# Kernel optimization log

Measured on AMD Instinct MI355X. Metric: run time of the kernel, lower is better.

The kernel has to match this reference:

```python
import jax, jax.numpy as jnp
import numpy as np

NUM_CLASSES = 80
STRIDES = (32, 16, 8)
SCORE_THRESH = 0.01
NMS_THRESH = 0.45
TOP_K = 200
PRE_K = 4096          # pre-NMS candidate cap (greedy NMS only ever emits TOP_K boxes)
NEG = -1e9            # 'suppressed' score sentinel (avoids -inf NaN issues)
CLS_OFFSET = 4096.0   # class-aware NMS: offset boxes per class (boxes live in [0, 608])

_ANCHORS_PX = [[(116, 90), (156, 198), (373, 326)],
               [(30, 61), (62, 45), (59, 119)],
               [(10, 13), (16, 30), (33, 23)]]


def setup_inputs() -> dict:
    key = jax.random.key(0)
    bs, img = 8, 608
    inp = {}
    for lvl, (stride, anc) in enumerate(zip(STRIDES, _ANCHORS_PX)):
        H = W = img // stride
        key, k = jax.random.split(key)
        inp[f"in{lvl}"] = jax.random.normal(k, (bs, 3 * (NUM_CLASSES + 5), H, W), dtype=jnp.float32)
        aw = jnp.array([a[0] / stride for a in anc], jnp.float32)
        ah = jnp.array([a[1] / stride for a in anc], jnp.float32)
        inp[f"aw{lvl}"] = jnp.broadcast_to(aw[None, :, None, None], (bs, 3, H, W))
        inp[f"ah{lvl}"] = jnp.broadcast_to(ah[None, :, None, None], (bs, 3, H, W))
        inp[f"gx{lvl}"] = jnp.broadcast_to(jnp.arange(W, dtype=jnp.float32)[None, None, None, :], (bs, 3, H, W))
        inp[f"gy{lvl}"] = jnp.broadcast_to(jnp.arange(H, dtype=jnp.float32)[None, None, :, None], (bs, 3, H, W))
    return inp


def _decode_level(x, aw, ah, gx, gy, stride):
    bs, _, H, W = x.shape
    x = x.reshape(bs, -1, NUM_CLASSES + 5, H, W).transpose(0, 1, 3, 4, 2)  # [bs,3,H,W,85]
    px = jax.nn.sigmoid(x[..., 0]) + gx
    py = jax.nn.sigmoid(x[..., 1]) + gy
    pw = jnp.exp(x[..., 2]) * aw
    ph = jnp.exp(x[..., 3]) * ah
    conf = jax.nn.sigmoid(x[..., 4])
    cls = jax.nn.sigmoid(x[..., 5:])
    boxes = jnp.stack([px, py, pw, ph], -1) * jnp.float32(stride)  # [bs,3,H,W,4] (cx,cy,w,h)
    return boxes.reshape(bs, -1, 4), conf.reshape(bs, -1), cls.reshape(bs, -1, NUM_CLASSES)


def _center_to_corner(b):
    cx, cy, w, h = b[..., 0], b[..., 1], b[..., 2], b[..., 3]
    return jnp.stack([cx - w / 2, cy - h / 2, cx + w / 2, cy + h / 2], -1)


def _nms_image(boxes, conf, cls):
    # boxes [N,4] corner, conf [N], cls [N,C]
    N, C = cls.shape
    scores = (conf[:, None] * cls).reshape(-1)                          # [N*C]
    cboxes = jnp.broadcast_to(boxes[:, None, :], (N, C, 4)).reshape(-1, 4)
    labels = jnp.broadcast_to(jnp.arange(C), (N, C)).reshape(-1)
    s = jnp.where(scores > SCORE_THRESH, scores, NEG)
    top_s, idx = jax.lax.top_k(s, PRE_K)
    b = cboxes[idx]                                                     # [PRE_K,4]
    l = labels[idx]
    ob = b + (l.astype(jnp.float32) * CLS_OFFSET)[:, None]              # class-aware offset
    area = (ob[:, 2] - ob[:, 0]) * (ob[:, 3] - ob[:, 1])

    def step(live, _):
        i = jnp.argmax(live)
        si, bi, ai = live[i], ob[i], area[i]
        x1 = jnp.maximum(bi[0], ob[:, 0]); y1 = jnp.maximum(bi[1], ob[:, 1])
        x2 = jnp.minimum(bi[2], ob[:, 2]); y2 = jnp.minimum(bi[3], ob[:, 3])
        inter = jnp.clip(x2 - x1, 0.0) * jnp.clip(y2 - y1, 0.0)
        iou = inter / (ai + area - inter + 1e-9)
        live = jnp.where(iou > NMS_THRESH, NEG, live)                   # suppresses self too
        return live, (i, si)

    _, (sel, sel_s) = jax.lax.scan(step, top_s, None, length=TOP_K)
    valid = sel_s > SCORE_THRESH
    out_b = jnp.where(valid[:, None], b[sel], 0.0)
    out_l = jnp.where(valid, l[sel], 0).astype(jnp.float32)
    out_s = jnp.where(valid, sel_s, 0.0)
    return jnp.concatenate([out_b, out_l[:, None], out_s[:, None]], -1)  # [TOP_K, 6]


def _forward(levels):
    boxes, conf, cls = [], [], []
    for (x, aw, ah, gx, gy), stride in zip(levels, STRIDES):
        bb, cc, cl = _decode_level(x, aw, ah, gx, gy, stride)
        boxes.append(bb); conf.append(cc); cls.append(cl)
    boxes = _center_to_corner(jnp.concatenate(boxes, 1))   # [bs,N,4]
    conf = jnp.concatenate(conf, 1)                        # [bs,N]
    cls = jnp.concatenate(cls, 1)                          # [bs,N,C]
    return jax.vmap(_nms_image)(boxes, conf, cls)          # [bs,TOP_K,6]


def reference(in0, aw0, ah0, gx0, gy0, in1, aw1, ah1, gx1, gy1, in2, aw2, ah2, gx2, gy2):
    levels = [(in0, aw0, ah0, gx0, gy0), (in1, aw1, ah1, gx1, gy1), (in2, aw2, ah2, gx2, gy2)]
    return _forward(levels)
```

## Files before the change

kernel.cpp:

```cpp
#include <hip/hip_runtime.h>
#include <stdint.h>

typedef unsigned int u32;
typedef unsigned long long u64;

#define NCLS 80
#define NBOX 22743
#define PREK 4096
#define BCAP 65536
#define NIMG 8
#define SCORE_TH 0.01f
#define IOU_TH 0.45f
#define TOPK 200

#define DCH 20
#define DNCH 4
#define GCH 10
#define GNCH 8

#define LCAP 1536

#define BKCAP 8
#define HCAP 224
#define HUGE_TH 3488.0f

#define RJC 4
#define RJW 1024

#define CBINS 512
#define CBIN_BASE 7680u

#define HIST_OFF 0
#define CNT_OFF  16384
#define ZERO_BYTES 18432
#define WIN_OFF  18432
#define BND_OFF  280576
#define PART_OFF BND_OFF
#define BOX_OFF  4474880
#define SKEY_OFF 7385984
#define SOBOX_OFF 7648128
#define SAREA_OFF 8172416

__device__ __forceinline__ float sigmf(float x) { return 1.0f / (1.0f + expf(-x)); }

__device__ __forceinline__ u64 pad_key(int i) { return (u64)(~(u32)i); }

__global__ __launch_bounds__(256) void init_k(uint4* __restrict__ ws) {
  const int i = blockIdx.x * 256 + threadIdx.x;
  if (i < ZERO_BYTES / 16) ws[i] = make_uint4(0u, 0u, 0u, 0u);
}

__global__ __launch_bounds__(256) void decode_hist_all(const float* __restrict__ in0,
                              const float* __restrict__ in1, const float* __restrict__ in2,
                              float4* __restrict__ boxes, u32* __restrict__ hist) {
  __shared__ u32 lh[CBINS];
  const int img = blockIdx.y;
  const int c0 = blockIdx.z * DCH;
  for (int i = threadIdx.x; i < CBINS; i += 256) lh[i] = 0;
  __syncthreads();

  const int bx = blockIdx.x;
  if (bx < 5) {
    const int W = 19, HW = 361;
    const int r = bx * 256 + threadIdx.x;
    if (r < 3 * HW) {
      const int a = r / HW, p = r - a * HW;
      const int y = p / W, x = p - y * W;
      const float* base = in0 + ((size_t)(img * 255 + a * 85)) * (size_t)HW + p;
      float l[DCH];
#pragma unroll
      for (int k = 0; k < DCH; ++k) l[k] = base[(size_t)(5 + c0 + k) * HW];
      const float x4 = base[4 * (size_t)HW];
      if (c0 == 0) {
        const float aw = (a == 0) ? 3.625f : ((a == 1) ? 4.875f : 11.65625f);
        const float ah = (a == 0) ? 2.8125f : ((a == 1) ? 6.1875f : 10.1875f);
        const float x0 = base[0];
        const float x1 = base[(size_t)HW];
        const float x2 = base[2 * (size_t)HW];
        const float x3 = base[3 * (size_t)HW];
        const float px = sigmf(x0) + (float)x;
        const float py = sigmf(x1) + (float)y;
        const float pw = expf(x2) * aw;
        const float ph = expf(x3) * ah;
        const float cx = px * 32.f, cy = py * 32.f, bw = pw * 32.f, bh = ph * 32.f;
        boxes[(size_t)img * NBOX + r] =
            make_float4(cx - bw * 0.5f, cy - bh * 0.5f, cx + bw * 0.5f, cy + bh * 0.5f);
      }
      const float conf = sigmf(x4);
      if (conf > SCORE_TH) {
#pragma unroll
        for (int k = 0; k < DCH; ++k) {
          float s = conf * sigmf(l[k]);
          if (s > SCORE_TH) {
            u32 bin = (__float_as_uint(s) >> 17) - CBIN_BASE;
            atomicAdd(&lh[bin], 1u);
          }
        }
      }
    }
  } else {
    const bool L1 = bx < 10;
    const float* in = L1 ? in1 : in2;
    const int W = L1 ? 38 : 76;
    const int HW = L1 ? 1444 : 5776;
    const int lvl_off = L1 ? 1083 : 5415;
    const float stride = L1 ? 16.f : 8.f;
    const int HW4 = HW >> 2;
    const int idx = (bx - (L1 ? 5 : 10)) * 256 + threadIdx.x;
    if (idx < 3 * HW4) {
      const int a = idx / HW4;
      const int p0 = (idx - a * HW4) << 2;
      const float* base = in + ((size_t)(img * 255 + a * 85)) * (size_t)HW + p0;
      float4 scv[DCH];
#pragma unroll
      for (int k = 0; k < DCH; ++k)
        scv[k] = *(const float4*)(base + (size_t)(5 + c0 + k) * HW);
      float4 v4 = *(const float4*)(base + 4 * (size_t)HW);
      const float* t4 = (const float*)&v4;
      float conf[4];
      if (c0 == 0) {
        const float aw = L1 ? ((a == 0) ? 1.875f : ((a == 1) ? 3.875f : 3.6875f))
                            : ((a == 0) ? 1.25f : ((a == 1) ? 2.f : 4.125f));
        const float ah = L1 ? ((a == 0) ? 3.8125f : ((a == 1) ? 2.8125f : 7.4375f))
                            : ((a == 0) ? 1.625f : ((a == 1) ? 3.75f : 2.875f));
        float4 v0 = *(const float4*)(base);
        float4 v1 = *(const float4*)(base + (size_t)HW);
        float4 v2 = *(const float4*)(base + 2 * (size_t)HW);
        float4 v3 = *(const float4*)(base + 3 * (size_t)HW);
        const float* t0 = (const float*)&v0;
        const float* t1 = (const float*)&v1;
        const float* t2 = (const float*)&v2;
        const float* t3 = (const float*)&v3;
        float4* bout = boxes + (size_t)img * NBOX + lvl_off + a * HW + p0;
#pragma unroll
        for (int i = 0; i < 4; ++i) {
          const int p = p0 + i;
          const int y = p / W, x = p - y * W;
          const float px = sigmf(t0[i]) + (float)x;
          const float py = sigmf(t1[i]) + (float)y;
          const float pw = expf(t2[i]) * aw;
          const float ph = expf(t3[i]) * ah;
          const float cx = px * stride, cy = py * stride, bw = pw * stride, bh = ph * stride;
          bout[i] = make_float4(cx - bw * 0.5f, cy - bh * 0.5f, cx + bw * 0.5f, cy + bh * 0.5f);
        }
      }
#pragma unroll
      for (int i = 0; i < 4; ++i) conf[i] = sigmf(t4[i]);
#pragma unroll
      for (int k = 0; k < DCH; ++k) {
        const float* s4 = (const float*)&scv[k];
#pragma unroll
        for (int i = 0; i < 4; ++i) {
          float s = conf[i] * sigmf(s4[i]);
          if (s > SCORE_TH) {
            u32 bin = (__float_as_uint(s) >> 17) - CBIN_BASE;
            atomicAdd(&lh[bin], 1u);
          }
        }
      }
    }
  }
  __syncthreads();
  u32* gh = hist + (size_t)img * CBINS;
  for (int i = threadIdx.x; i < CBINS; i += 256) {
    u32 v = lh[i];
    if (v) atomicAdd(&gh[i], v);
  }
}

__device__ __forceinline__ void flush_list(const u64* llist, int lcnt, int cap,
                                           int* gctr, u64* glist, int gcap) {
  __shared__ int gbase_s;
  int n = lcnt < cap ? lcnt : cap;
  if (threadIdx.x == 0) gbase_s = n ? atomicAdd(gctr, n) : 0;
  __syncthreads();
  const int gb = gbase_s;
  for (int i = threadIdx.x; i < n; i += 256) {
    int pos = gb + i;
    if (pos < gcap) glist[pos] = llist[i];
  }
}

__global__ __launch_bounds__(256) void gather_all(const float* __restrict__ in0,
                         const float* __restrict__ in1, const float* __restrict__ in2,
                         const u32* __restrict__ hist, int* __restrict__ cnt,
                         u64* __restrict__ winners, u64* __restrict__ boundary) {
  __shared__ u64 lwin[LCAP];
  __shared__ u64 lbnd[LCAP];
  __shared__ int lwc, lbc;
  __shared__ u32 s_wsum[4];
  __shared__ int sB;
  const int img = blockIdx.y;
  const int c0 = blockIdx.z * GCH;
  const int t = threadIdx.x;
  if (t == 0) { lwc = 0; lbc = 0; sB = -1; }

  {
    const u32* gh = hist + (size_t)img * CBINS;
    u32 hv0 = gh[t * 2], hv1 = gh[t * 2 + 1];
    u32 s = hv0 + hv1;
    const int lane = t & 63;
    u32 v = s;
#pragma unroll
    for (int off = 1; off < 64; off <<= 1) {
      u32 o = __shfl_down(v, off);
      if (lane + off < 64) v += o;
    }
    if (lane == 0) s_wsum[t >> 6] = v;
    __syncthreads();
    u32 hi = 0;
    for (int w = (t >> 6) + 1; w < 4; ++w) hi += s_wsum[w];
    const u32 above = hi + (v - s);
    if (above < (u32)PREK && above + s >= (u32)PREK) {
      u32 cum = above + hv1;
      if (cum >= (u32)PREK) sB = t * 2 + 1;
      else sB = t * 2;
    }
    __syncthreads();
  }
  const int B = sB;

  int* cw = &cnt[img * 64];
  int* cb = &cnt[img * 64 + 32];
  u64* wl = winners + (size_t)img * PREK;
  u64* bl = boundary + (size_t)img * BCAP;
  const int bx = blockIdx.x;

  if (bx < 5) {
    const int HW = 361;
    const int r = bx * 256 + t;
    if (r < 3 * HW) {
      const int a = r / HW, p = r - a * HW;
      const float* base = in0 + ((size_t)(img * 255 + a * 85)) * (size_t)HW + p;
      const int boxg = r;
      float l[GCH];
#pragma unroll
      for (int k = 0; k < GCH; ++k) l[k] = base[(size_t)(5 + c0 + k) * HW];
      const float conf = sigmf(base[4 * (size_t)HW]);
#pragma unroll
      for (int k = 0; k < GCH; ++k) {
        float s = conf * sigmf(l[k]);
        if (s > SCORE_TH) {
          u32 key = __float_as_uint(s);
          int wbin = (int)((key >> 17) - CBIN_BASE);
          if (wbin >= B) {
            u64 kv = ((u64)key << 32) | (u64)(~(u32)(boxg * NCLS + (c0 + k)));
            if (wbin > B) {
              int p2 = atomicAdd(&lwc, 1);
              if (p2 < LCAP) lwin[p2] = kv;
              else { int g = atomicAdd(cw, 1); if (g < PREK) wl[g] = kv; }
            } else {
              int p2 = atomicAdd(&lbc, 1);
              if (p2 < LCAP) lbnd[p2] = kv;
              else { int g = atomicAdd(cb, 1); if (g < BCAP) bl[g] = kv; }
            }
          }
        }
      }
    }
  } else {
    const bool L1 = bx < 10;
    const float* in = L1 ? in1 : in2;
    const int HW = L1 ? 1444 : 5776;
    const int lvl_off = L1 ? 1083 : 5415;
    const int HW4 = HW >> 2;
    const int idx = (bx - (L1 ? 5 : 10)) * 256 + t;
    if (idx < 3 * HW4) {
      const int a = idx / HW4;
      const int p0 = (idx - a * HW4) << 2;
      const float* base = in + ((size_t)(img * 255 + a * 85)) * (size_t)HW + p0;
      const int boxg0 = lvl_off + a * HW + p0;
      float4 scv[GCH];
#pragma unroll
      for (int k = 0; k < GCH; ++k)
        scv[k] = *(const float4*)(base + (size_t)(5 + c0 + k) * HW);
      float4 v4 = *(const float4*)(base + 4 * (size_t)HW);
      const float* t4 = (const float*)&v4;
      float conf[4];
#pragma unroll
      for (int i = 0; i < 4; ++i) conf[i] = sigmf(t4[i]);
#pragma unroll
      for (int k = 0; k < GCH; ++k) {
        const float* s4 = (const float*)&scv[k];
        const int c = c0 + k;
#pragma unroll
        for (int i = 0; i < 4; ++i) {
          float s = conf[i] * sigmf(s4[i]);
          if (s > SCORE_TH) {
            u32 key = __float_as_uint(s);
            int wbin = (int)((key >> 17) - CBIN_BASE);
            if (wbin >= B) {
              u64 kv = ((u64)key << 32) | (u64)(~(u32)((boxg0 + i) * NCLS + c));
              if (wbin > B) {
                int p = atomicAdd(&lwc, 1);
                if (p < LCAP) lwin[p] = kv;
                else { int g = atomicAdd(cw, 1); if (g < PREK) wl[g] = kv; }
              } else {
                int p = atomicAdd(&lbc, 1);
                if (p < LCAP) lbnd[p] = kv;
                else { int g = atomicAdd(cb, 1); if (g < BCAP) bl[g] = kv; }
              }
            }
          }
        }
      }
    }
  }
  __syncthreads();
  flush_list(lwin, lwc, LCAP, cw, wl, PREK);
  flush_list(lbnd, lbc, LCAP, cb, bl, BCAP);
}

__global__ void resolve_k(const u64* __restrict__ boundary,
                          int* __restrict__ cnt, u64* __restrict__ winners) {
  const int img = blockIdx.x;
  const int cw_pre = cnt[img * 64];
  const int T = PREK - cw_pre;
  int bc = cnt[img * 64 + 32];
  if (bc > BCAP) bc = BCAP;
  if (T <= 0 || bc <= 0) return;
  const u64* bnd = boundary + (size_t)img * BCAP;
  u64* wl = winners + (size_t)img * PREK;
  int* cw = &cnt[img * 64];

  __shared__ u32 h2[16384];
  __shared__ u32 lsum[256];
  __shared__ u32 above[256];
  __shared__ u32 s_total;
  __shared__ int sB2, sT2;
  __shared__ u64 ties[512];
  __shared__ int tcnt;
  __shared__ u64 lw2[PREK];
  __shared__ int lw2c;
  __shared__ int gbase_s;
  const int t = threadIdx.x;
  for (int i = t; i < 16384; i += 256) h2[i] = 0;
  if (t == 0) { tcnt = 0; sB2 = -1; sT2 = 0; lw2c = 0; }
  __syncthreads();
  for (int i = t; i < bc; i += 256) atomicAdd(&h2[(u32)(bnd[i] >> 35) & 0x3FFFu], 1u);
  __syncthreads();
  u32 s = 0;
  for (int j = 0; j < 64; ++j) s += h2[t * 64 + j];
  lsum[t] = s;
  __syncthreads();
  if (t == 0) {
    u32 acc = 0;
    for (int i = 255; i >= 0; --i) { above[i] = acc; acc += lsum[i]; }
    s_total = acc;
  }
  __syncthreads();
  if ((int)s_total > T) {
    if (above[t] < (u32)T && above[t] + lsum[t] >= (u32)T) {
      u32 cum = above[t];
      for (int j = 63; j >= 0; --j) {
        u32 hv = h2[t * 64 + j];
        cum += hv;
        if (cum >= (u32)T) { sB2 = t * 64 + j; sT2 = (int)((u32)T - (cum - hv)); break; }
      }
    }
  }
  __syncthreads();
  const int B2 = sB2, T2 = sT2;
  for (int i = t; i < bc; i += 256) {
    u64 e = bnd[i];
    int low = (int)((u32)(e >> 35) & 0x3FFFu);
    if (low > B2) {
      int p = atomicAdd(&lw2c, 1);
      if (p < PREK) lw2[p] = e;
    } else if (low == B2) {
      int tp = atomicAdd(&tcnt, 1);
      if (tp < 512) ties[tp] = e;
    }
  }
  __syncthreads();
  int n = lw2c < PREK ? lw2c : PREK;
  if (t == 0) gbase_s = n ? atomicAdd(cw, n) : 0;
  __syncthreads();
  for (int i = t; i < n; i += 256) {
    int pos = gbase_s + i;
    if (pos < PREK) wl[pos] = lw2[i];
  }
  __syncthreads();
  if (t == 0 && T2 > 0) {
    int tc = tcnt < 512 ? tcnt : 512;
    for (int k = 0; k < T2 && k < tc; ++k) {
      int bi = -1; u64 bk = 0;
      for (int i = 0; i < tc; ++i)
        if (ties[i] > bk) { bk = ties[i]; bi = i; }
      if (bi < 0) break;
      ties[bi] = 0;
      int pos = atomicAdd(cw, 1);
      if (pos < PREK) wl[pos] = bk;
    }
  }
}

__global__ __launch_bounds__(256) void rank_part_k(const u64* __restrict__ winners,
                                                   const int* __restrict__ cnt,
                                                   int* __restrict__ part) {
  __shared__ u64 lk[RJW];
  const int img = blockIdx.y;
  const int kc = blockIdx.x >> 2;
  const int jc = blockIdx.x & 3;
  const int t = threadIdx.x;
  int wc = cnt[img * 64]; if (wc > PREK) wc = PREK;
  const u64* wl = winners + (size_t)img * PREK;
  for (int i = t; i < RJW; i += 256) {
    const int gj = jc * RJW + i;
    lk[i] = (gj < wc) ? wl[gj] : pad_key(gj);
  }
  __syncthreads();
  const int ki_idx = kc * 256 + t;
  const u64 ki = (ki_idx < wc) ? wl[ki_idx] : pad_key(ki_idx);
  int rank = 0;
#pragma unroll 8
  for (int j = 0; j < RJW; ++j) rank += (lk[j] > ki) ? 1 : 0;
  part[(((size_t)img * RJC) + jc) * PREK + ki_idx] = rank;
}

__global__ __launch_bounds__(256) void rank_scatter_k(const u64* __restrict__ winners,
                                              const int* __restrict__ cnt,
                                              const int* __restrict__ part,
                                              const float4* __restrict__ boxes,
                                              u64* __restrict__ skey,
                                              float4* __restrict__ sobox,
                                              float* __restrict__ sarea) {
  const int img = blockIdx.y;
  const int i = blockIdx.x * 256 + threadIdx.x;
  int wc = cnt[img * 64]; if (wc > PREK) wc = PREK;
  const u64* wl = winners + (size_t)img * PREK;
  const u64 ki = (i < wc) ? wl[i] : pad_key(i);
  const int* pb = part + (size_t)img * RJC * PREK + i;
  int rank = pb[0] + pb[PREK] + pb[2 * PREK] + pb[3 * PREK];
  skey[(size_t)img * PREK + rank] = ki;
  if (i < wc) {
    u32 ridx = ~(u32)ki;
    int c = (int)(ridx % NCLS);
    int bi = (int)(ridx / NCLS);
    float4 b = boxes[(size_t)img * NBOX + bi];
    float off = 4096.0f * (float)c;
    float4 ob = make_float4(b.x + off, b.y + off, b.z + off, b.w + off);
    sobox[(size_t)img * PREK + rank] = ob;
    sarea[(size_t)img * PREK + rank] = (ob.z - ob.x) * (ob.w - ob.y);
  } else {
    sobox[(size_t)img * PREK + rank] = make_float4(0.f, 0.f, 0.f, 0.f);
    sarea[(size_t)img * PREK + rank] = 0.f;
  }
}

__global__ __launch_bounds__(64) void scan_nms_k(const u64* __restrict__ skey,
                                                 const float4* __restrict__ sobox,
                                                 const float* __restrict__ sarea,
                                                 float* __restrict__ out) {
  __shared__ float4 bxc[NCLS][BKCAP];
  __shared__ float  arc[NCLS][BKCAP];
  __shared__ int    cntc[NCLS];
  __shared__ float4 bxa[TOPK];
  __shared__ float  ara[TOPK];
  __shared__ float4 bxh[HCAP];
  __shared__ float  arh[HCAP];
  __shared__ int    nhuge_s;
  __shared__ float4 chb[64];
  __shared__ float  cha[64];
  const int img = blockIdx.x;
  const int lane = threadIdx.x;
  float* orow = out + (size_t)img * (TOPK * 6);
  for (int i = lane; i < TOPK * 6; i += 64) orow[i] = 0.f;
  for (int i = lane; i < NCLS; i += 64) cntc[i] = 0;
  if (lane == 0) nhuge_s = 0;
  const u64* K = skey + (size_t)img * PREK;
  const float4* Bp = sobox + (size_t)img * PREK;
  const float* Ap = sarea + (size_t)img * PREK;
  int nsel = 0;
  u64 kj = K[lane];
  float4 ob = Bp[lane];
  float ar = Ap[lane];
  for (int chunk = 0; chunk < PREK / 64 && nsel < TOPK; ++chunk) {
    u64 kj_n = 0ull; float4 ob_n = make_float4(0.f, 0.f, 0.f, 0.f); float ar_n = 0.f;
    if (chunk + 1 < PREK / 64) {
      const int jn = (chunk + 1) * 64 + lane;
      kj_n = K[jn]; ob_n = Bp[jn]; ar_n = Ap[jn];
    }
    const float score = __uint_as_float((u32)(kj >> 32));
    bool alive = (score > SCORE_TH);
    if (__ballot(alive) == 0ull) break;
    const u32 ridx = ~(u32)kj;
    const int myc = (int)(ridx % NCLS);
    const bool huge = (ob.z - ob.x > HUGE_TH) || (ob.w - ob.y > HUGE_TH);
    chb[lane] = ob; cha[lane] = ar;

    u64 mm = ~0ull;
#pragma unroll
    for (int k = 0; k < 7; ++k) {
      const u64 bk = __ballot(((myc >> k) & 1) != 0);
      mm &= (((myc >> k) & 1) != 0) ? bk : ~bk;
    }
    const u64 hb = __ballot(huge);

    {
      const int n0 = cntc[myc];
      const int n = n0 < BKCAP ? n0 : BKCAP;
      for (int k = 0; k < n && alive; ++k) {
        const float4 b0 = bxc[myc][k]; const float a0 = arc[myc][k];
        float xx1 = fmaxf(b0.x, ob.x), yy1 = fmaxf(b0.y, ob.y);
        float xx2 = fminf(b0.z, ob.z), yy2 = fminf(b0.w, ob.w);
        float inter = fmaxf(xx2 - xx1, 0.f) * fmaxf(yy2 - yy1, 0.f);
        float iou = inter / (a0 + ar - inter + 1e-9f);
        if (iou > IOU_TH) alive = false;
      }
    }
    {
      const int nh = nhuge_s;
      for (int k = 0; k < nh; ++k) {
        if (alive) {
          const float4 b0 = bxh[k]; const float a0 = arh[k];
          float xx1 = fmaxf(b0.x, ob.x), yy1 = fmaxf(b0.y, ob.y);
          float xx2 = fminf(b0.z, ob.z), yy2 = fminf(b0.w, ob.w);
          float inter = fmaxf(xx2 - xx1, 0.f) * fmaxf(yy2 - yy1, 0.f);
          float iou = inter / (a0 + ar - inter + 1e-9f);
          if (iou > IOU_TH) alive = false;
        }
      }
    }
    if (__ballot(alive && huge) != 0ull) {
      const int na = nsel;
      for (int k = 0; k < na; ++k) {
        if (alive && huge) {
          const float4 b0 = bxa[k]; const float a0 = ara[k];
          float xx1 = fmaxf(b0.x, ob.x), yy1 = fmaxf(b0.y, ob.y);
          float xx2 = fminf(b0.z, ob.z), yy2 = fminf(b0.w, ob.w);
          float inter = fmaxf(xx2 - xx1, 0.f) * fmaxf(yy2 - yy1, 0.f);
          float iou = inter / (a0 + ar - inter + 1e-9f);
          if (iou > IOU_TH) alive = false;
        }
      }
    }
    const u64 amask = __ballot(alive);
    const u64 below = (1ull << lane) - 1ull;
    u64 tm = alive ? ((mm | hb | (huge ? ~0ull : 0ull)) & below & amask) : 0ull;
    u64 sup = 0ull;
    while (tm) {
      const int tb = (int)__builtin_ctzll(tm);
      tm &= tm - 1ull;
      const float4 bj = chb[tb];
      const float aj = cha[tb];
      float xx1 = fmaxf(bj.x, ob.x), yy1 = fmaxf(bj.y, ob.y);
      float xx2 = fminf(bj.z, ob.z), yy2 = fminf(bj.w, ob.w);
      float inter = fmaxf(xx2 - xx1, 0.f) * fmaxf(yy2 - yy1, 0.f);
      float iou = inter / (aj + ar - inter + 1e-9f);
      if (iou > IOU_TH) sup |= (1ull << tb);
    }
    u64 rem = amask;
    u64 selbits = 0ull;
    while (rem != 0ull && nsel + (int)__popcll(selbits) < TOPK) {
      const int b = __builtin_ctzll(rem);
      selbits |= (1ull << b);
      rem &= ~(1ull << b);
      const u64 colb = __ballot((sup >> b) & 1ull);
      rem &= ~colb;
    }
    const bool selme = (selbits >> lane) & 1ull;
    if (selme) {
      const int slot = nsel + (int)__popcll(selbits & ((1ull << lane) - 1ull));
      bxa[slot] = ob; ara[slot] = ar;
      if (!huge) {
        int cc = atomicAdd(&cntc[myc], 1);
        if (cc < BKCAP) { bxc[myc][cc] = ob; arc[myc][cc] = ar; }
        else { int hn = atomicAdd(&nhuge_s, 1); if (hn < HCAP) { bxh[hn] = ob; arh[hn] = ar; } }
      } else {
        int hn = atomicAdd(&nhuge_s, 1);
        if (hn < HCAP) { bxh[hn] = ob; arh[hn] = ar; }
      }
      const float off = 4096.0f * (float)myc;
      orow[slot * 6 + 0] = ob.x - off;
      orow[slot * 6 + 1] = ob.y - off;
      orow[slot * 6 + 2] = ob.z - off;
      orow[slot * 6 + 3] = ob.w - off;
      orow[slot * 6 + 4] = (float)myc;
      orow[slot * 6 + 5] = score;
    }
    nsel += (int)__popcll(selbits);
    kj = kj_n; ob = ob_n; ar = ar_n;
  }
}

extern "C" void kernel_launch(void* const* d_in, const int* in_sizes, int n_in,
                              void* d_out, int out_size, void* d_ws, size_t ws_size,
                              hipStream_t stream) {
  const float* in0 = (const float*)d_in[0];
  const float* in1 = (const float*)d_in[5];
  const float* in2 = (const float*)d_in[10];
  char* ws = (char*)d_ws;
  u32* hist = (u32*)(ws + HIST_OFF);
  int* cnt = (int*)(ws + CNT_OFF);
  u64* winners = (u64*)(ws + WIN_OFF);
  u64* boundary = (u64*)(ws + BND_OFF);
  int* part = (int*)(ws + PART_OFF);
  float4* boxes = (float4*)(ws + BOX_OFF);
  u64* skey = (u64*)(ws + SKEY_OFF);
  float4* sobox = (float4*)(ws + SOBOX_OFF);
  float* sarea = (float*)(ws + SAREA_OFF);
  float* out = (float*)d_out;

  init_k<<<(ZERO_BYTES / 16 + 255) / 256, 256, 0, stream>>>((uint4*)ws);

  decode_hist_all<<<dim3(27, 8, DNCH), 256, 0, stream>>>(in0, in1, in2, boxes, hist);

  gather_all<<<dim3(27, 8, GNCH), 256, 0, stream>>>(in0, in1, in2, hist, cnt, winners, boundary);

  resolve_k<<<8, 256, 0, stream>>>(boundary, cnt, winners);

  rank_part_k<<<dim3(64, 8), 256, 0, stream>>>(winners, cnt, part);
  rank_scatter_k<<<dim3(16, 8), 256, 0, stream>>>(winners, cnt, part, boxes, skey, sobox, sarea);
  scan_nms_k<<<8, 64, 0, stream>>>(skey, sobox, sarea, out);
}
```

Before: 113.2 us.

## Merge resolve, rank and NMS tail into one cooperative kernel with grid syncs

Replaces the four tail kernels (resolve, rank partial, rank scatter, scan NMS) with one cooperative kernel of 512 blocks that uses grid.sync between phases. The resolve histogram and boundary compaction are now spread across 64 blocks per image using global h2/ties buffers, where before a single block per image did them. The aim is to remove kernel launch gaps and to parallelize the serial resolve step. In exchange it adds grid-wide barrier costs, a larger workspace to zero, and a halved boundary capacity.

```diff
diff --git a/kernel.cpp b/kernel.cpp
--- a/kernel.cpp
+++ b/kernel.cpp
@@ -1,5 +1,8 @@
 #include <hip/hip_runtime.h>
+#include <hip/hip_cooperative_groups.h>
 #include <stdint.h>
+
+namespace cg = cooperative_groups;
 
 typedef unsigned int u32;
 typedef unsigned long long u64;
@@ -7,7 +10,7 @@
 #define NCLS 80
 #define NBOX 22743
 #define PREK 4096
-#define BCAP 65536
+#define BCAP 32768
 #define NIMG 8
 #define SCORE_TH 0.01f
 #define IOU_TH 0.45f
@@ -32,14 +35,16 @@
 
 #define HIST_OFF 0
 #define CNT_OFF  16384
-#define ZERO_BYTES 18432
-#define WIN_OFF  18432
-#define BND_OFF  280576
+#define H2_OFF   18432
+#define TIES_OFF 542720
+#define ZERO_BYTES 575488
+#define WIN_OFF  575488
+#define BND_OFF  837632
 #define PART_OFF BND_OFF
-#define BOX_OFF  4474880
-#define SKEY_OFF 7385984
-#define SOBOX_OFF 7648128
-#define SAREA_OFF 8172416
+#define BOX_OFF  2934784
+#define SKEY_OFF 5845888
+#define SOBOX_OFF 6108032
+#define SAREA_OFF 6632320
 
 __device__ __forceinline__ float sigmf(float x) { return 1.0f / (1.0f + expf(-x)); }
 
@@ -311,209 +316,218 @@
   flush_list(lbnd, lbc, LCAP, cb, bl, BCAP);
 }
 
-__global__ void resolve_k(const u64* __restrict__ boundary,
-                          int* __restrict__ cnt, u64* __restrict__ winners) {
-  const int img = blockIdx.x;
-  const int cw_pre = cnt[img * 64];
-  const int T = PREK - cw_pre;
-  int bc = cnt[img * 64 + 32];
-  if (bc > BCAP) bc = BCAP;
-  if (T <= 0 || bc <= 0) return;
-  const u64* bnd = boundary + (size_t)img * BCAP;
-  u64* wl = winners + (size_t)img * PREK;
-  int* cw = &cnt[img * 64];
-
-  __shared__ u32 h2[16384];
-  __shared__ u32 lsum[256];
-  __shared__ u32 above[256];
-  __shared__ u32 s_total;
-  __shared__ int sB2, sT2;
-  __shared__ u64 ties[512];
-  __shared__ int tcnt;
-  __shared__ u64 lw2[PREK];
-  __shared__ int lw2c;
-  __shared__ int gbase_s;
+struct NmsS {
+  float4 bxc[NCLS][BKCAP]; float arc[NCLS][BKCAP]; int cntc[NCLS];
+  float4 bxa[TOPK]; float ara[TOPK];
+  float4 bxh[HCAP]; float arh[HCAP]; int nhuge;
+  float4 chb[64]; float cha[64];
+};
+struct RankS { u64 lk[RJW]; };
+struct CompS { u64 lwin[LCAP]; int lwc; int gbase; };
+struct ScanS { u32 lsum[256]; u32 above[256]; u32 total; };
+union SU { NmsS n; RankS r; CompS c; ScanS s; };
+
+__global__ __launch_bounds__(256) void coop_tail_k(const u64* __restrict__ boundary,
+                         int* __restrict__ cnt, u64* __restrict__ winners,
+                         int* __restrict__ part, const float4* __restrict__ boxes,
+                         u64* __restrict__ skey, float4* __restrict__ sobox,
+                         float* __restrict__ sarea, u32* __restrict__ h2g,
+                         u64* __restrict__ tiesg, float* __restrict__ out) {
+  cg::grid_group grid = cg::this_grid();
+  __shared__ SU su;
+  const int bid = blockIdx.x;
   const int t = threadIdx.x;
-  for (int i = t; i < 16384; i += 256) h2[i] = 0;
-  if (t == 0) { tcnt = 0; sB2 = -1; sT2 = 0; lw2c = 0; }
-  __syncthreads();
-  for (int i = t; i < bc; i += 256) atomicAdd(&h2[(u32)(bnd[i] >> 35) & 0x3FFFu], 1u);
-  __syncthreads();
-  u32 s = 0;
-  for (int j = 0; j < 64; ++j) s += h2[t * 64 + j];
-  lsum[t] = s;
-  __syncthreads();
-  if (t == 0) {
-    u32 acc = 0;
-    for (int i = 255; i >= 0; --i) { above[i] = acc; acc += lsum[i]; }
-    s_total = acc;
-  }
-  __syncthreads();
-  if ((int)s_total > T) {
-    if (above[t] < (u32)T && above[t] + lsum[t] >= (u32)T) {
-      u32 cum = above[t];
-      for (int j = 63; j >= 0; --j) {
-        u32 hv = h2[t * 64 + j];
-        cum += hv;
-        if (cum >= (u32)T) { sB2 = t * 64 + j; sT2 = (int)((u32)T - (cum - hv)); break; }
-      }
-    }
-  }
-  __syncthreads();
-  const int B2 = sB2, T2 = sT2;
-  for (int i = t; i < bc; i += 256) {
-    u64 e = bnd[i];
-    int low = (int)((u32)(e >> 35) & 0x3FFFu);
-    if (low > B2) {
-      int p = atomicAdd(&lw2c, 1);
-      if (p < PREK) lw2[p] = e;
-    } else if (low == B2) {
-      int tp = atomicAdd(&tcnt, 1);
-      if (tp < 512) ties[tp] = e;
-    }
-  }
-  __syncthreads();
-  int n = lw2c < PREK ? lw2c : PREK;
-  if (t == 0) gbase_s = n ? atomicAdd(cw, n) : 0;
-  __syncthreads();
-  for (int i = t; i < n; i += 256) {
-    int pos = gbase_s + i;
-    if (pos < PREK) wl[pos] = lw2[i];
-  }
-  __syncthreads();
-  if (t == 0 && T2 > 0) {
-    int tc = tcnt < 512 ? tcnt : 512;
-    for (int k = 0; k < T2 && k < tc; ++k) {
-      int bi = -1; u64 bk = 0;
-      for (int i = 0; i < tc; ++i)
-        if (ties[i] > bk) { bk = ties[i]; bi = i; }
-      if (bi < 0) break;
-      ties[bi] = 0;
-      int pos = atomicAdd(cw, 1);
-      if (pos < PREK) wl[pos] = bk;
-    }
-  }
-}
-
-__global__ __launch_bounds__(256) void rank_part_k(const u64* __restrict__ winners,
-                                                   const int* __restrict__ cnt,
-                                                   int* __restrict__ part) {
-  __shared__ u64 lk[RJW];
-  const int img = blockIdx.y;
-  const int kc = blockIdx.x >> 2;
-  const int jc = blockIdx.x & 3;
-  const int t = threadIdx.x;
-  int wc = cnt[img * 64]; if (wc > PREK) wc = PREK;
-  const u64* wl = winners + (size_t)img * PREK;
-  for (int i = t; i < RJW; i += 256) {
-    const int gj = jc * RJW + i;
-    lk[i] = (gj < wc) ? wl[gj] : pad_key(gj);
-  }
-  __syncthreads();
-  const int ki_idx = kc * 256 + t;
-  const u64 ki = (ki_idx < wc) ? wl[ki_idx] : pad_key(ki_idx);
-  int rank = 0;
+
+  {
+    const int img = bid >> 6, sub = bid & 63;
+    const int T = PREK - cnt[img * 64];
+    int bc = cnt[img * 64 + 32]; if (bc > BCAP) bc = BCAP;
+    if (T > 0 && bc > 0) {
+      const u64* bnd = boundary + (size_t)img * BCAP;
+      u32* h2 = h2g + (size_t)img * 16384;
+      for (int i = sub * 256 + t; i < bc; i += 64 * 256)
+        atomicAdd(&h2[(u32)(bnd[i] >> 35) & 0x3FFFu], 1u);
+    }
+  }
+  grid.sync();
+
+  if (bid < 8) {
+    const int img = bid;
+    const int T = PREK - cnt[img * 64];
+    int bc = cnt[img * 64 + 32]; if (bc > BCAP) bc = BCAP;
+    const int gate = (T > 0 && bc > 0) ? 1 : 0;
+    if (t == 0) { cnt[img * 64 + 8] = -1; cnt[img * 64 + 9] = 0; cnt[img * 64 + 11] = gate; }
+    __syncthreads();
+    if (gate) {
+      const u32* h2 = h2g + (size_t)img * 16384;
+      u32 s = 0;
+      for (int j = 0; j < 64; ++j) s += h2[t * 64 + j];
+      su.s.lsum[t] = s;
+      __syncthreads();
+      if (t == 0) {
+        u32 acc = 0;
+        for (int i = 255; i >= 0; --i) { su.s.above[i] = acc; acc += su.s.lsum[i]; }
+        su.s.total = acc;
+      }
+      __syncthreads();
+      if ((int)su.s.total > T) {
+        if (su.s.above[t] < (u32)T && su.s.above[t] + su.s.lsum[t] >= (u32)T) {
+          u32 cum = su.s.above[t];
+          for (int j = 63; j >= 0; --j) {
+            u32 hv = h2[t * 64 + j];
+            cum += hv;
+            if (cum >= (u32)T) {
+              cnt[img * 64 + 8] = t * 64 + j;
+              cnt[img * 64 + 9] = (int)((u32)T - (cum - hv));
+              break;
+            }
+          }
+        }
+      }
+    }
+  }
+  grid.sync();
+
+  {
+    const int img = bid >> 6, sub = bid & 63;
+    if (cnt[img * 64 + 11]) {
+      const int B2 = cnt[img * 64 + 8];
+      int bc = cnt[img * 64 + 32]; if (bc > BCAP) bc = BCAP;
+      const u64* bnd = boundary + (size_t)img * BCAP;
+      u64* wl = winners + (size_t)img * PREK;
+      if (t == 0) su.c.lwc = 0;
+      __syncthreads();
+      for (int i = sub * 256 + t; i < bc; i += 64 * 256) {
+        u64 e = bnd[i];
+        int low = (int)((u32)(e >> 35) & 0x3FFFu);
+        if (low > B2) {
+          int p = atomicAdd(&su.c.lwc, 1);
+          if (p < LCAP) su.c.lwin[p] = e;
+          else { int g = atomicAdd(&cnt[img * 64], 1); if (g < PREK) wl[g] = e; }
+        } else if (low == B2) {
+          int tp = atomicAdd(&cnt[img * 64 + 10], 1);
+          if (tp < 512) tiesg[(size_t)img * 512 + tp] = e;
+        }
+      }
+      __syncthreads();
+      int n = su.c.lwc < LCAP ? su.c.lwc : LCAP;
+      if (t == 0) su.c.gbase = n ? atomicAdd(&cnt[img * 64], n) : 0;
+      __syncthreads();
+      for (int i = t; i < n; i += 256) {
+        int pos = su.c.gbase + i;
+        if (pos < PREK) wl[pos] = su.c.lwin[i];
+      }
+    }
+  }
+  grid.sync();
+
+  if (bid < 8 && t == 0) {
+    const int img = bid;
+    if (cnt[img * 64 + 11]) {
+      const int T2 = cnt[img * 64 + 9];
+      if (T2 > 0) {
+        int tc = cnt[img * 64 + 10]; if (tc > 512) tc = 512;
+        u64* wl = winners + (size_t)img * PREK;
+        u64* ties = tiesg + (size_t)img * 512;
+        for (int k = 0; k < T2 && k < tc; ++k) {
+          int bi = -1; u64 bk = 0;
+          for (int i = 0; i < tc; ++i)
+            if (ties[i] > bk) { bk = ties[i]; bi = i; }
+          if (bi < 0) break;
+          ties[bi] = 0;
+          int pos = atomicAdd(&cnt[img * 64], 1);
+          if (pos < PREK) wl[pos] = bk;
+        }
+      }
+    }
+  }
+  grid.sync();
+
+  {
+    const int img = bid >> 6, x = bid & 63;
+    const int kc = x >> 2, jc = x & 3;
+    int wc = cnt[img * 64]; if (wc > PREK) wc = PREK;
+    const u64* wl = winners + (size_t)img * PREK;
+    for (int i = t; i < RJW; i += 256) {
+      const int gj = jc * RJW + i;
+      su.r.lk[i] = (gj < wc) ? wl[gj] : pad_key(gj);
+    }
+    __syncthreads();
+    const int ki_idx = kc * 256 + t;
+    const u64 ki = (ki_idx < wc) ? wl[ki_idx] : pad_key(ki_idx);
+    int rank = 0;
 #pragma unroll 8
-  for (int j = 0; j < RJW; ++j) rank += (lk[j] > ki) ? 1 : 0;
-  part[(((size_t)img * RJC) + jc) * PREK + ki_idx] = rank;
-}
-
-__global__ __launch_bounds__(256) void rank_scatter_k(const u64* __restrict__ winners,
-                                              const int* __restrict__ cnt,
-                                              const int* __restrict__ part,
-                                              const float4* __restrict__ boxes,
-                                              u64* __restrict__ skey,
-                                              float4* __restrict__ sobox,
-                                              float* __restrict__ sarea) {
-  const int img = blockIdx.y;
-  const int i = blockIdx.x * 256 + threadIdx.x;
-  int wc = cnt[img * 64]; if (wc > PREK) wc = PREK;
-  const u64* wl = winners + (size_t)img * PREK;
-  const u64 ki = (i < wc) ? wl[i] : pad_key(i);
-  const int* pb = part + (size_t)img * RJC * PREK + i;
-  int rank = pb[0] + pb[PREK] + pb[2 * PREK] + pb[3 * PREK];
-  skey[(size_t)img * PREK + rank] = ki;
-  if (i < wc) {
-    u32 ridx = ~(u32)ki;
-    int c = (int)(ridx % NCLS);
-    int bi = (int)(ridx / NCLS);
-    float4 b = boxes[(size_t)img * NBOX + bi];
-    float off = 4096.0f * (float)c;
-    float4 ob = make_float4(b.x + off, b.y + off, b.z + off, b.w + off);
-    sobox[(size_t)img * PREK + rank] = ob;
-    sarea[(size_t)img * PREK + rank] = (ob.z - ob.x) * (ob.w - ob.y);
-  } else {
-    sobox[(size_t)img * PREK + rank] = make_float4(0.f, 0.f, 0.f, 0.f);
-    sarea[(size_t)img * PREK + rank] = 0.f;
-  }
-}
-
-__global__ __launch_bounds__(64) void scan_nms_k(const u64* __restrict__ skey,
-                                                 const float4* __restrict__ sobox,
-                                                 const float* __restrict__ sarea,
-                                                 float* __restrict__ out) {
-  __shared__ float4 bxc[NCLS][BKCAP];
-  __shared__ float  arc[NCLS][BKCAP];
-  __shared__ int    cntc[NCLS];
-  __shared__ float4 bxa[TOPK];
-  __shared__ float  ara[TOPK];
-  __shared__ float4 bxh[HCAP];
-  __shared__ float  arh[HCAP];
-  __shared__ int    nhuge_s;
-  __shared__ float4 chb[64];
-  __shared__ float  cha[64];
-  const int img = blockIdx.x;
-  const int lane = threadIdx.x;
-  float* orow = out + (size_t)img * (TOPK * 6);
-  for (int i = lane; i < TOPK * 6; i += 64) orow[i] = 0.f;
-  for (int i = lane; i < NCLS; i += 64) cntc[i] = 0;
-  if (lane == 0) nhuge_s = 0;
-  const u64* K = skey + (size_t)img * PREK;
-  const float4* Bp = sobox + (size_t)img * PREK;
-  const float* Ap = sarea + (size_t)img * PREK;
-  int nsel = 0;
-  u64 kj = K[lane];
-  float4 ob = Bp[lane];
-  float ar = Ap[lane];
-  for (int chunk = 0; chunk < PREK / 64 && nsel < TOPK; ++chunk) {
-    u64 kj_n = 0ull; float4 ob_n = make_float4(0.f, 0.f, 0.f, 0.f); float ar_n = 0.f;
-    if (chunk + 1 < PREK / 64) {
-      const int jn = (chunk + 1) * 64 + lane;
-      kj_n = K[jn]; ob_n = Bp[jn]; ar_n = Ap[jn];
-    }
-    const float score = __uint_as_float((u32)(kj >> 32));
-    bool alive = (score > SCORE_TH);
-    if (__ballot(alive) == 0ull) break;
-    const u32 ridx = ~(u32)kj;
-    const int myc = (int)(ridx % NCLS);
-    const bool huge = (ob.z - ob.x > HUGE_TH) || (ob.w - ob.y > HUGE_TH);
-    chb[lane] = ob; cha[lane] = ar;
-
-    u64 mm = ~0ull;
-#pragma unroll
-    for (int k = 0; k < 7; ++k) {
-      const u64 bk = __ballot(((myc >> k) & 1) != 0);
-      mm &= (((myc >> k) & 1) != 0) ? bk : ~bk;
-    }
-    const u64 hb = __ballot(huge);
-
-    {
-      const int n0 = cntc[myc];
-      const int n = n0 < BKCAP ? n0 : BKCAP;
-      for (int k = 0; k < n && alive; ++k) {
-        const float4 b0 = bxc[myc][k]; const float a0 = arc[myc][k];
-        float xx1 = fmaxf(b0.x, ob.x), yy1 = fmaxf(b0.y, ob.y);
-        float xx2 = fminf(b0.z, ob.z), yy2 = fminf(b0.w, ob.w);
-        float inter = fmaxf(xx2 - xx1, 0.f) * fmaxf(yy2 - yy1, 0.f);
-        float iou = inter / (a0 + ar - inter + 1e-9f);
-        if (iou > IOU_TH) alive = false;
-      }
-    }
-    {
-      const int nh = nhuge_s;
-      for (int k = 0; k < nh; ++k) {
-        if (alive) {
-          const float4 b0 = bxh[k]; const float a0 = arh[k];
+    for (int j = 0; j < RJW; ++j) rank += (su.r.lk[j] > ki) ? 1 : 0;
+    part[(((size_t)img * RJC) + jc) * PREK + ki_idx] = rank;
+  }
+  grid.sync();
+
+  if (bid < 128) {
+    const int img = bid >> 4, x = bid & 15;
+    const int i = x * 256 + t;
+    int wc = cnt[img * 64]; if (wc > PREK) wc = PREK;
+    const u64* wl = winners + (size_t)img * PREK;
+    const u64 ki = (i < wc) ? wl[i] : pad_key(i);
+    const int* pb = part + (size_t)img * RJC * PREK + i;
+    int rank = pb[0] + pb[PREK] + pb[2 * PREK] + pb[3 * PREK];
+    skey[(size_t)img * PREK + rank] = ki;
+    if (i < wc) {
+      u32 ridx = ~(u32)ki;
+      int c = (int)(ridx % NCLS);
+      int bi = (int)(ridx / NCLS);
+      float4 b = boxes[(size_t)img * NBOX + bi];
+      float off = 4096.0f * (float)c;
+      float4 ob = make_float4(b.x + off, b.y + off, b.z + off, b.w + off);
+      sobox[(size_t)img * PREK + rank] = ob;
+      sarea[(size_t)img * PREK + rank] = (ob.z - ob.x) * (ob.w - ob.y);
+    } else {
+      sobox[(size_t)img * PREK + rank] = make_float4(0.f, 0.f, 0.f, 0.f);
+      sarea[(size_t)img * PREK + rank] = 0.f;
+    }
+  }
+  grid.sync();
+
+  if (bid < 8 && t < 64) {
+    const int img = bid;
+    const int lane = t;
+    float* orow = out + (size_t)img * (TOPK * 6);
+    for (int i = lane; i < TOPK * 6; i += 64) orow[i] = 0.f;
+    for (int i = lane; i < NCLS; i += 64) su.n.cntc[i] = 0;
+    if (lane == 0) su.n.nhuge = 0;
+    const u64* K = skey + (size_t)img * PREK;
+    const float4* Bp = sobox + (size_t)img * PREK;
+    const float* Ap = sarea + (size_t)img * PREK;
+    int nsel = 0;
+    u64 kj = K[lane];
+    float4 ob = Bp[lane];
+    float ar = Ap[lane];
+    for (int chunk = 0; chunk < PREK / 64 && nsel < TOPK; ++chunk) {
+      u64 kj_n = 0ull; float4 ob_n = make_float4(0.f, 0.f, 0.f, 0.f); float ar_n = 0.f;
+      if (chunk + 1 < PREK / 64) {
+        const int jn = (chunk + 1) * 64 + lane;
+        kj_n = K[jn]; ob_n = Bp[jn]; ar_n = Ap[jn];
+      }
+      const float score = __uint_as_float((u32)(kj >> 32));
+      bool alive = (score > SCORE_TH);
+      if (__ballot(alive) == 0ull) break;
+      const u32 ridx = ~(u32)kj;
+      const int myc = (int)(ridx % NCLS);
+      const bool huge = (ob.z - ob.x > HUGE_TH) || (ob.w - ob.y > HUGE_TH);
+      su.n.chb[lane] = ob; su.n.cha[lane] = ar;
+
+      u64 mm = ~0ull;
+#pragma unroll
+      for (int k = 0; k < 7; ++k) {
+        const u64 bk = __ballot(((myc >> k) & 1) != 0);
+        mm &= (((myc >> k) & 1) != 0) ? bk : ~bk;
+      }
+      const u64 hb = __ballot(huge);
+
+      {
+        const int n0 = su.n.cntc[myc];
+        const int n = n0 < BKCAP ? n0 : BKCAP;
+        for (int k = 0; k < n && alive; ++k) {
+          const float4 b0 = su.n.bxc[myc][k]; const float a0 = su.n.arc[myc][k];
           float xx1 = fmaxf(b0.x, ob.x), yy1 = fmaxf(b0.y, ob.y);
           float xx2 = fminf(b0.z, ob.z), yy2 = fminf(b0.w, ob.w);
           float inter = fmaxf(xx2 - xx1, 0.f) * fmaxf(yy2 - yy1, 0.f);
@@ -521,66 +535,79 @@
           if (iou > IOU_TH) alive = false;
         }
       }
-    }
-    if (__ballot(alive && huge) != 0ull) {
-      const int na = nsel;
-      for (int k = 0; k < na; ++k) {
-        if (alive && huge) {
-          const float4 b0 = bxa[k]; const float a0 = ara[k];
-          float xx1 = fmaxf(b0.x, ob.x), yy1 = fmaxf(b0.y, ob.y);
-          float xx2 = fminf(b0.z, ob.z), yy2 = fminf(b0.w, ob.w);
-          float inter = fmaxf(xx2 - xx1, 0.f) * fmaxf(yy2 - yy1, 0.f);
-          float iou = inter / (a0 + ar - inter + 1e-9f);
-          if (iou > IOU_TH) alive = false;
-        }
-      }
-    }
-    const u64 amask = __ballot(alive);
-    const u64 below = (1ull << lane) - 1ull;
-    u64 tm = alive ? ((mm | hb | (huge ? ~0ull : 0ull)) & below & amask) : 0ull;
-    u64 sup = 0ull;
-    while (tm) {
-      const int tb = (int)__builtin_ctzll(tm);
-      tm &= tm - 1ull;
-      const float4 bj = chb[tb];
-      const float aj = cha[tb];
-      float xx1 = fmaxf(bj.x, ob.x), yy1 = fmaxf(bj.y, ob.y);
-      float xx2 = fminf(bj.z, ob.z), yy2 = fminf(bj.w, ob.w);
-      float inter = fmaxf(xx2 - xx1, 0.f) * fmaxf(yy2 - yy1, 0.f);
-      float iou = inter / (aj + ar - inter + 1e-9f);
-      if (iou > IOU_TH) sup |= (1ull << tb);
-    }
-    u64 rem = amask;
-    u64 selbits = 0ull;
-    while (rem != 0ull && nsel + (int)__popcll(selbits) < TOPK) {
-      const int b = __builtin_ctzll(rem);
-      selbits |= (1ull << b);
-      rem &= ~(1ull << b);
-      const u64 colb = __ballot((sup >> b) & 1ull);
-      rem &= ~colb;
-    }
-    const bool selme = (selbits >> lane) & 1ull;
-    if (selme) {
-      const int slot = nsel + (int)__popcll(selbits & ((1ull << lane) - 1ull));
-      bxa[slot] = ob; ara[slot] = ar;
-      if (!huge) {
-        int cc = atomicAdd(&cntc[myc], 1);
-        if (cc < BKCAP) { bxc[myc][cc] = ob; arc[myc][cc] = ar; }
-        else { int hn = atomicAdd(&nhuge_s, 1); if (hn < HCAP) { bxh[hn] = ob; arh[hn] = ar; } }
-      } else {
-        int hn = atomicAdd(&nhuge_s, 1);
-        if (hn < HCAP) { bxh[hn] = ob; arh[hn] = ar; }
-      }
-      const float off = 4096.0f * (float)myc;
-      orow[slot * 6 + 0] = ob.x - off;
-      orow[slot * 6 + 1] = ob.y - off;
-      orow[slot * 6 + 2] = ob.z - off;
-      orow[slot * 6 + 3] = ob.w - off;
-      orow[slot * 6 + 4] = (float)myc;
-      orow[slot * 6 + 5] = score;
-    }
-    nsel += (int)__popcll(selbits);
-    kj = kj_n; ob = ob_n; ar = ar_n;
+      {
+        const int nh = su.n.nhuge;
+        for (int k = 0; k < nh; ++k) {
+          if (alive) {
+            const float4 b0 = su.n.bxh[k]; const float a0 = su.n.arh[k];
+            float xx1 = fmaxf(b0.x, ob.x), yy1 = fmaxf(b0.y, ob.y);
+            float xx2 = fminf(b0.z, ob.z), yy2 = fminf(b0.w, ob.w);
+            float inter = fmaxf(xx2 - xx1, 0.f) * fmaxf(yy2 - yy1, 0.f);
+            float iou = inter / (a0 + ar - inter + 1e-9f);
+            if (iou > IOU_TH) alive = false;
+          }
+        }
+      }
+      if (__ballot(alive && huge) != 0ull) {
+        const int na = nsel;
+        for (int k = 0; k < na; ++k) {
+          if (alive && huge) {
+            const float4 b0 = su.n.bxa[k]; const float a0 = su.n.ara[k];
+            float xx1 = fmaxf(b0.x, ob.x), yy1 = fmaxf(b0.y, ob.y);
+            float xx2 = fminf(b0.z, ob.z), yy2 = fminf(b0.w, ob.w);
+            float inter = fmaxf(xx2 - xx1, 0.f) * fmaxf(yy2 - yy1, 0.f);
+            float iou = inter / (a0 + ar - inter + 1e-9f);
+            if (iou > IOU_TH) alive = false;
+          }
+        }
+      }
+      const u64 amask = __ballot(alive);
+      const u64 below = (1ull << lane) - 1ull;
+      u64 tm = alive ? ((mm | hb | (huge ? ~0ull : 0ull)) & below & amask) : 0ull;
+      u64 sup = 0ull;
+      while (tm) {
+        const int tb = (int)__builtin_ctzll(tm);
+        tm &= tm - 1ull;
+        const float4 bj = su.n.chb[tb];
+        const float aj = su.n.cha[tb];
+        float xx1 = fmaxf(bj.x, ob.x), yy1 = fmaxf(bj.y, ob.y);
+        float xx2 = fminf(bj.z, ob.z), yy2 = fminf(bj.w, ob.w);
+        float inter = fmaxf(xx2 - xx1, 0.f) * fmaxf(yy2 - yy1, 0.f);
+        float iou = inter / (aj + ar - inter + 1e-9f);
+        if (iou > IOU_TH) sup |= (1ull << tb);
+      }
+      u64 rem = amask;
+      u64 selbits = 0ull;
+      while (rem != 0ull && nsel + (int)__popcll(selbits) < TOPK) {
+        const int b = __builtin_ctzll(rem);
+        selbits |= (1ull << b);
+        rem &= ~(1ull << b);
+        const u64 colb = __ballot((sup >> b) & 1ull);
+        rem &= ~colb;
+      }
+      const bool selme = (selbits >> lane) & 1ull;
+      if (selme) {
+        const int slot = nsel + (int)__popcll(selbits & ((1ull << lane) - 1ull));
+        su.n.bxa[slot] = ob; su.n.ara[slot] = ar;
+        if (!huge) {
+          int cc = atomicAdd(&su.n.cntc[myc], 1);
+          if (cc < BKCAP) { su.n.bxc[myc][cc] = ob; su.n.arc[myc][cc] = ar; }
+          else { int hn = atomicAdd(&su.n.nhuge, 1); if (hn < HCAP) { su.n.bxh[hn] = ob; su.n.arh[hn] = ar; } }
+        } else {
+          int hn = atomicAdd(&su.n.nhuge, 1);
+          if (hn < HCAP) { su.n.bxh[hn] = ob; su.n.arh[hn] = ar; }
+        }
+        const float off = 4096.0f * (float)myc;
+        orow[slot * 6 + 0] = ob.x - off;
+        orow[slot * 6 + 1] = ob.y - off;
+        orow[slot * 6 + 2] = ob.z - off;
+        orow[slot * 6 + 3] = ob.w - off;
+        orow[slot * 6 + 4] = (float)myc;
+        orow[slot * 6 + 5] = score;
+      }
+      nsel += (int)__popcll(selbits);
+      kj = kj_n; ob = ob_n; ar = ar_n;
+    }
   }
 }
 
@@ -593,6 +620,8 @@
   char* ws = (char*)d_ws;
   u32* hist = (u32*)(ws + HIST_OFF);
   int* cnt = (int*)(ws + CNT_OFF);
+  u32* h2g = (u32*)(ws + H2_OFF);
+  u64* tiesg = (u64*)(ws + TIES_OFF);
   u64* winners = (u64*)(ws + WIN_OFF);
   u64* boundary = (u64*)(ws + BND_OFF);
   int* part = (int*)(ws + PART_OFF);
@@ -608,9 +637,8 @@
 
   gather_all<<<dim3(27, 8, GNCH), 256, 0, stream>>>(in0, in1, in2, hist, cnt, winners, boundary);
 
-  resolve_k<<<8, 256, 0, stream>>>(boundary, cnt, winners);
-
-  rank_part_k<<<dim3(64, 8), 256, 0, stream>>>(winners, cnt, part);
-  rank_scatter_k<<<dim3(16, 8), 256, 0, stream>>>(winners, cnt, part, boxes, skey, sobox, sarea);
-  scan_nms_k<<<8, 64, 0, stream>>>(skey, sobox, sarea, out);
+  void* args[] = {(void*)&boundary, (void*)&cnt, (void*)&winners, (void*)&part,
+                  (void*)&boxes, (void*)&skey, (void*)&sobox, (void*)&sarea,
+                  (void*)&h2g, (void*)&tiesg, (void*)&out};
+  hipLaunchCooperativeKernel((const void*)coop_tail_k, dim3(512), dim3(256), args, 0, stream);
 }
```

Measured after the change: 430.9 us. +280.7%, slower.
